# Optimization experiments

Measured on AMD Instinct MI355X. Metric: run time of the kernel, lower is better.

The kernel has to match this reference:

```python
import jax, jax.numpy as jnp
import numpy as np

N = 10000       # n_nodes
E = 640000      # n_edges (avg degree 64)
D_IN = 128      # in_feats
D_H = 128       # n_hidden
N_CLS = 64      # n_classes


def setup_inputs() -> dict:
    key = jax.random.key(0)
    k1, k2, k3, k4, k5, k6 = jax.random.split(key, 6)
    features = jax.random.normal(k1, (N, D_IN), dtype=jnp.float32)
    src = jax.random.randint(k2, (E,), 0, N, dtype=jnp.int32)
    dst = jax.random.randint(k3, (E,), 0, N, dtype=jnp.int32)
    s = 0.05  # small init scale to keep activations bounded across 3 layers
    # Stored as [in, out]; equivalent to torch Linear weight [out, in] transposed.
    W0 = jax.random.normal(k4, (D_IN, D_H), dtype=jnp.float32) * s
    W1 = jax.random.normal(k5, (D_H, D_H), dtype=jnp.float32) * s
    W2 = jax.random.normal(k6, (D_H, N_CLS), dtype=jnp.float32) * s
    return {"features": features, "W0": W0, "W1": W1, "W2": W2,
            "src": src, "dst": dst}


def reference(features, W0, W1, W2, src, dst):
    # GINConv with aggregator 'sum', eps=0 (learn_eps=False):
    #   h' = Linear(h + sum_{(u->v) in E} h[u] scattered to v)
    # Dropout is identity at inference; 'activation' is unused in the module.
    def gin_layer(h, W):
        agg = jax.ops.segment_sum(h[src], dst, num_segments=N)  # [N, d]
        return (h + agg) @ W

    h = gin_layer(features, W0)
    h = gin_layer(h, W1)
    h = gin_layer(h, W2)
    return h
```

## Files before the change

### kernel.cpp

```cpp
#include <hip/hip_runtime.h>
#include <hip/hip_bf16.h>

#define NN 10000
#define NE 640000
#define D_IN 128
#define D_H 128
#define N_CLS 64
#define CAP 160
#define GRP 157
#define CAPC 4800
#define EPB 1024
#define AB 625
#define CB 1251
#define CCS 16

__device__ __forceinline__ float blo(unsigned u) { return __uint_as_float(u << 16); }
__device__ __forceinline__ float bhi(unsigned u) { return __uint_as_float(u & 0xffff0000u); }
__device__ __forceinline__ unsigned short f2bf(float f) {
    unsigned u = __float_as_uint(f);
    return (unsigned short)((u + 0x7fffu + ((u >> 16) & 1u)) >> 16);
}

__global__ __launch_bounds__(256) void prep_a(const int* __restrict__ src,
                                              const int* __restrict__ dst,
                                              int* __restrict__ coarse_cnt,
                                              unsigned* __restrict__ coarse,
                                              const float* __restrict__ feat,
                                              unsigned* __restrict__ hb0) {
    int bid = blockIdx.x;
    if (bid >= AB) {
        int t = (bid - AB) * 256 + threadIdx.x;
        if (t < NN * 32) {
            float4 f = ((const float4*)feat)[t];
            unsigned lo = (unsigned)f2bf(f.x) | ((unsigned)f2bf(f.y) << 16);
            unsigned hi = (unsigned)f2bf(f.z) | ((unsigned)f2bf(f.w) << 16);
            ((uint2*)hb0)[t] = make_uint2(lo, hi);
        } else if (t < (NN + 1) * 32) {
            ((uint2*)hb0)[t] = make_uint2(0u, 0u);
        }
        return;
    }
    __shared__ unsigned stage[EPB];
    __shared__ int hist[GRP], gbase[GRP], cur[GRP];
    const int t = threadIdx.x;
    for (int i = t; i < GRP; i += 256) hist[i] = 0;
    __syncthreads();
    const int e0 = bid * EPB;
    for (int i = t; i < EPB; i += 256) {
        int s = src[e0 + i];
        int d = dst[e0 + i];
        stage[i] = (unsigned)s | ((unsigned)d << 16);
        atomicAdd(&hist[d >> 6], 1);
    }
    __syncthreads();
    for (int i = t; i < GRP; i += 256) {
        gbase[i] = atomicAdd(&coarse_cnt[i * CCS], hist[i]);
        cur[i] = 0;
    }
    __syncthreads();
    for (int i = t; i < EPB; i += 256) {
        unsigned u = stage[i];
        int g = u >> 22;
        int r = atomicAdd(&cur[g], 1);
        coarse[g * CAPC + gbase[g] + r] = u;
    }
}

__global__ __launch_bounds__(1024) void prep_b(const int* __restrict__ coarse_cnt,
                                               const unsigned* __restrict__ coarse,
                                               int* __restrict__ cnt,
                                               unsigned short* __restrict__ colbuf) {
    __shared__ int cur[64];
    const int g = blockIdx.x;
    const int t = threadIdx.x;
    if (t < 64) cur[t] = 0;
    __syncthreads();
    const int m = coarse_cnt[g * CCS];
    const unsigned* cb = coarse + g * CAPC;
    for (int i = t; i < m; i += 1024) {
        unsigned u = cb[i];
        int s = (int)(u & 0xFFFFu);
        int d = (int)(u >> 16);
        int r = atomicAdd(&cur[d - (g << 6)], 1);
        colbuf[d * CAP + r] = (unsigned short)s;
    }
    __syncthreads();
    if (t < 64) {
        int n = (g << 6) + t;
        if (n < NN) {
            int c = cur[t];
            int pad = (4 - (c & 3)) & 3;
            unsigned short* base = colbuf + n * CAP;
            for (int k = 0; k < pad; ++k) base[c + k] = (unsigned short)NN;
            cnt[n] = c + pad;
        }
    }
}

template <int J, int M, bool LAST>
__global__ __launch_bounds__(256) void gin_layer(const uint4* __restrict__ hb4,
                                                 const int* __restrict__ cnt,
                                                 const unsigned short* __restrict__ colbuf,
                                                 const float* __restrict__ W,
                                                 unsigned short* __restrict__ outb,
                                                 float* __restrict__ outf) {
    __shared__ float xs[M][D_H];
    const int base = blockIdx.x * M;
    const int tid = threadIdx.x;
    const int wave = tid >> 6;
    const int lane = tid & 63;
    const int sub = lane >> 4;
    const int off = lane & 15;

#pragma unroll 1
    for (int nm = 0; nm < M / 4; ++nm) {
        const int m = wave + nm * 4;
        const int n = base + m;
        float a0, a1, a2, a3, a4, a5, a6, a7;
        if (sub == 0) {
            uint4 u = hb4[n * 16 + off];
            a0 = blo(u.x); a1 = bhi(u.x); a2 = blo(u.y); a3 = bhi(u.y);
            a4 = blo(u.z); a5 = bhi(u.z); a6 = blo(u.w); a7 = bhi(u.w);
        } else {
            a0 = a1 = a2 = a3 = a4 = a5 = a6 = a7 = 0.f;
        }
        const int G4 = cnt[n] >> 2;
        const uint2* cl8 = (const uint2*)(colbuf + n * CAP);
        int g = 0;
        for (; g + 4 <= G4; g += 4) {
            uint2 p0 = cl8[g + 0];
            uint2 p1 = cl8[g + 1];
            uint2 p2 = cl8[g + 2];
            uint2 p3 = cl8[g + 3];
            unsigned w0 = (sub & 2) ? p0.y : p0.x;
            unsigned w1 = (sub & 2) ? p1.y : p1.x;
            unsigned w2 = (sub & 2) ? p2.y : p2.x;
            unsigned w3 = (sub & 2) ? p3.y : p3.x;
            int s0 = (sub & 1) ? (w0 >> 16) : (w0 & 0xffffu);
            int s1 = (sub & 1) ? (w1 >> 16) : (w1 & 0xffffu);
            int s2 = (sub & 1) ? (w2 >> 16) : (w2 & 0xffffu);
            int s3 = (sub & 1) ? (w3 >> 16) : (w3 & 0xffffu);
            uint4 uA = hb4[s0 * 16 + off];
            uint4 uB = hb4[s1 * 16 + off];
            uint4 uC = hb4[s2 * 16 + off];
            uint4 uD = hb4[s3 * 16 + off];
            a0 += (blo(uA.x) + blo(uB.x)) + (blo(uC.x) + blo(uD.x));
            a1 += (bhi(uA.x) + bhi(uB.x)) + (bhi(uC.x) + bhi(uD.x));
            a2 += (blo(uA.y) + blo(uB.y)) + (blo(uC.y) + blo(uD.y));
            a3 += (bhi(uA.y) + bhi(uB.y)) + (bhi(uC.y) + bhi(uD.y));
            a4 += (blo(uA.z) + blo(uB.z)) + (blo(uC.z) + blo(uD.z));
            a5 += (bhi(uA.z) + bhi(uB.z)) + (bhi(uC.z) + bhi(uD.z));
            a6 += (blo(uA.w) + blo(uB.w)) + (blo(uC.w) + blo(uD.w));
            a7 += (bhi(uA.w) + bhi(uB.w)) + (bhi(uC.w) + bhi(uD.w));
        }
        for (; g < G4; ++g) {
            uint2 p = cl8[g];
            unsigned w = (sub & 2) ? p.y : p.x;
            int s = (sub & 1) ? (w >> 16) : (w & 0xffffu);
            uint4 u = hb4[s * 16 + off];
            a0 += blo(u.x); a1 += bhi(u.x); a2 += blo(u.y); a3 += bhi(u.y);
            a4 += blo(u.z); a5 += bhi(u.z); a6 += blo(u.w); a7 += bhi(u.w);
        }
        a0 += __shfl_xor(a0, 16); a0 += __shfl_xor(a0, 32);
        a1 += __shfl_xor(a1, 16); a1 += __shfl_xor(a1, 32);
        a2 += __shfl_xor(a2, 16); a2 += __shfl_xor(a2, 32);
        a3 += __shfl_xor(a3, 16); a3 += __shfl_xor(a3, 32);
        a4 += __shfl_xor(a4, 16); a4 += __shfl_xor(a4, 32);
        a5 += __shfl_xor(a5, 16); a5 += __shfl_xor(a5, 32);
        a6 += __shfl_xor(a6, 16); a6 += __shfl_xor(a6, 32);
        a7 += __shfl_xor(a7, 16); a7 += __shfl_xor(a7, 32);
        if (sub == 0) {
            *(float4*)&xs[m][8 * off]     = make_float4(a0, a1, a2, a3);
            *(float4*)&xs[m][8 * off + 4] = make_float4(a4, a5, a6, a7);
        }
    }
    __syncthreads();

    constexpr int G = 256 / J;
    constexpr int NM = M / G;
    const int gq = tid / J;
    const int j = tid % J;
    const int mbase = gq * NM;
    float acc[NM];
#pragma unroll
    for (int m = 0; m < NM; ++m) acc[m] = 0.f;

    for (int k = 0; k < D_H; k += 4) {
        float w0 = W[(k + 0) * J + j];
        float w1 = W[(k + 1) * J + j];
        float w2 = W[(k + 2) * J + j];
        float w3 = W[(k + 3) * J + j];
#pragma unroll
        for (int m = 0; m < NM; ++m) {
            float4 xv = *(const float4*)&xs[mbase + m][k];
            acc[m] += xv.x * w0 + xv.y * w1 + xv.z * w2 + xv.w * w3;
        }
    }
#pragma unroll
    for (int m = 0; m < NM; ++m) {
        int n = base + mbase + m;
        if (LAST) __builtin_nontemporal_store(acc[m], &outf[(size_t)n * J + j]);
        else      __builtin_nontemporal_store(f2bf(acc[m]), &outb[(size_t)n * J + j]);
    }
    if (!LAST && blockIdx.x == 0 && tid < 32) {
        ((uint2*)(outb + (size_t)NN * D_H))[tid] = make_uint2(0u, 0u);
    }
}

extern "C" void kernel_launch(void* const* d_in, const int* in_sizes, int n_in,
                              void* d_out, int out_size, void* d_ws, size_t ws_size,
                              hipStream_t stream) {
    const float* features = (const float*)d_in[0];
    const float* W0       = (const float*)d_in[1];
    const float* W1       = (const float*)d_in[2];
    const float* W2       = (const float*)d_in[3];
    const int*   src      = (const int*)d_in[4];
    const int*   dst      = (const int*)d_in[5];
    float* out = (float*)d_out;

    int* coarse_cnt        = (int*)d_ws;
    int* cnt               = coarse_cnt + GRP * CCS;
    unsigned short* colbuf = (unsigned short*)(cnt + NN);
    unsigned* coarse       = (unsigned*)(colbuf + (size_t)NN * CAP);
    unsigned* hb0          = coarse + (size_t)GRP * CAPC;
    unsigned* hb1          = hb0 + (size_t)(NN + 1) * 64;
    unsigned* hb2          = hb1 + (size_t)(NN + 1) * 64;

    hipMemsetAsync(coarse_cnt, 0, GRP * CCS * sizeof(int), stream);
    prep_a<<<AB + CB, 256, 0, stream>>>(src, dst, coarse_cnt, coarse, features, hb0);
    prep_b<<<GRP, 1024, 0, stream>>>(coarse_cnt, coarse, cnt, colbuf);

    constexpr int M = 8;
    gin_layer<D_H, M, false><<<NN / M, 256, 0, stream>>>((const uint4*)hb0, cnt, colbuf, W0,
                                                         (unsigned short*)hb1, nullptr);
    gin_layer<D_H, M, false><<<NN / M, 256, 0, stream>>>((const uint4*)hb1, cnt, colbuf, W1,
                                                         (unsigned short*)hb2, nullptr);
    gin_layer<N_CLS, M, true><<<NN / M, 256, 0, stream>>>((const uint4*)hb2, cnt, colbuf, W2,
                                                          nullptr, out);
}
```

Before: 147.6 us.

## Use bf16-packed weights, one node per wave, and pad neighbor lists to 16

Weights are pre-packed into bf16 pairs inside the prep kernel, which halves weight load traffic in each layer's matmul. Each GIN layer block now handles 4 nodes (one per wave) instead of 8, giving 2500 blocks and requesting higher occupancy through launch bounds. Neighbor lists are padded to multiples of 16 so the unrolled gather loop needs no remainder loop. The trade-offs are more dummy-row gathers, more blocks each reloading the weight matrix, and bf16 rounding of the weights, which adds precision loss.

```diff
diff --git a/kernel.cpp b/kernel.cpp
--- a/kernel.cpp
+++ b/kernel.cpp
@@ -12,6 +12,7 @@
 #define EPB 1024
 #define AB 625
 #define CB 1251
+#define WB 80
 #define CCS 16
 
 __device__ __forceinline__ float blo(unsigned u) { return __uint_as_float(u << 16); }
@@ -20,21 +21,44 @@
     unsigned u = __float_as_uint(f);
     return (unsigned short)((u + 0x7fffu + ((u >> 16) & 1u)) >> 16);
 }
+__device__ __forceinline__ unsigned packbf(float a, float b) {
+    return (unsigned)f2bf(a) | ((unsigned)f2bf(b) << 16);
+}
 
 __global__ __launch_bounds__(256) void prep_a(const int* __restrict__ src,
                                               const int* __restrict__ dst,
                                               int* __restrict__ coarse_cnt,
                                               unsigned* __restrict__ coarse,
                                               const float* __restrict__ feat,
-                                              unsigned* __restrict__ hb0) {
+                                              unsigned* __restrict__ hb0,
+                                              const float* __restrict__ W0,
+                                              const float* __restrict__ W1,
+                                              const float* __restrict__ W2,
+                                              unsigned* __restrict__ wb0,
+                                              unsigned* __restrict__ wb1,
+                                              unsigned* __restrict__ wb2) {
     int bid = blockIdx.x;
+    if (bid >= AB + CB) {
+        int t = (bid - AB - CB) * 256 + threadIdx.x;
+        if (t < 8192) {
+            int kp = t >> 7, j = t & 127;
+            wb0[t] = packbf(W0[(2 * kp) * 128 + j], W0[(2 * kp + 1) * 128 + j]);
+        } else if (t < 16384) {
+            int tt = t - 8192;
+            int kp = tt >> 7, j = tt & 127;
+            wb1[tt] = packbf(W1[(2 * kp) * 128 + j], W1[(2 * kp + 1) * 128 + j]);
+        } else if (t < 20480) {
+            int tt = t - 16384;
+            int kp = tt >> 6, j = tt & 63;
+            wb2[tt] = packbf(W2[(2 * kp) * 64 + j], W2[(2 * kp + 1) * 64 + j]);
+        }
+        return;
+    }
     if (bid >= AB) {
         int t = (bid - AB) * 256 + threadIdx.x;
         if (t < NN * 32) {
             float4 f = ((const float4*)feat)[t];
-            unsigned lo = (unsigned)f2bf(f.x) | ((unsigned)f2bf(f.y) << 16);
-            unsigned hi = (unsigned)f2bf(f.z) | ((unsigned)f2bf(f.w) << 16);
-            ((uint2*)hb0)[t] = make_uint2(lo, hi);
+            ((uint2*)hb0)[t] = make_uint2(packbf(f.x, f.y), packbf(f.z, f.w));
         } else if (t < (NN + 1) * 32) {
             ((uint2*)hb0)[t] = make_uint2(0u, 0u);
         }
@@ -89,7 +113,7 @@
         int n = (g << 6) + t;
         if (n < NN) {
             int c = cur[t];
-            int pad = (4 - (c & 3)) & 3;
+            int pad = (16 - (c & 15)) & 15;
             unsigned short* base = colbuf + n * CAP;
             for (int k = 0; k < pad; ++k) base[c + k] = (unsigned short)NN;
             cnt[n] = c + pad;
@@ -97,13 +121,14 @@
     }
 }
 
-template <int J, int M, bool LAST>
-__global__ __launch_bounds__(256) void gin_layer(const uint4* __restrict__ hb4,
-                                                 const int* __restrict__ cnt,
-                                                 const unsigned short* __restrict__ colbuf,
-                                                 const float* __restrict__ W,
-                                                 unsigned short* __restrict__ outb,
-                                                 float* __restrict__ outf) {
+template <int J, bool LAST>
+__global__ __launch_bounds__(256, 8) void gin_layer(const uint4* __restrict__ hb4,
+                                                    const int* __restrict__ cnt,
+                                                    const unsigned short* __restrict__ colbuf,
+                                                    const unsigned* __restrict__ Wb,
+                                                    unsigned short* __restrict__ outb,
+                                                    float* __restrict__ outf) {
+    constexpr int M = 4;
     __shared__ float xs[M][D_H];
     const int base = blockIdx.x * M;
     const int tid = threadIdx.x;
@@ -112,67 +137,54 @@
     const int sub = lane >> 4;
     const int off = lane & 15;
 
-#pragma unroll 1
-    for (int nm = 0; nm < M / 4; ++nm) {
-        const int m = wave + nm * 4;
-        const int n = base + m;
-        float a0, a1, a2, a3, a4, a5, a6, a7;
-        if (sub == 0) {
-            uint4 u = hb4[n * 16 + off];
-            a0 = blo(u.x); a1 = bhi(u.x); a2 = blo(u.y); a3 = bhi(u.y);
-            a4 = blo(u.z); a5 = bhi(u.z); a6 = blo(u.w); a7 = bhi(u.w);
-        } else {
-            a0 = a1 = a2 = a3 = a4 = a5 = a6 = a7 = 0.f;
-        }
-        const int G4 = cnt[n] >> 2;
-        const uint2* cl8 = (const uint2*)(colbuf + n * CAP);
-        int g = 0;
-        for (; g + 4 <= G4; g += 4) {
-            uint2 p0 = cl8[g + 0];
-            uint2 p1 = cl8[g + 1];
-            uint2 p2 = cl8[g + 2];
-            uint2 p3 = cl8[g + 3];
-            unsigned w0 = (sub & 2) ? p0.y : p0.x;
-            unsigned w1 = (sub & 2) ? p1.y : p1.x;
-            unsigned w2 = (sub & 2) ? p2.y : p2.x;
-            unsigned w3 = (sub & 2) ? p3.y : p3.x;
-            int s0 = (sub & 1) ? (w0 >> 16) : (w0 & 0xffffu);
-            int s1 = (sub & 1) ? (w1 >> 16) : (w1 & 0xffffu);
-            int s2 = (sub & 1) ? (w2 >> 16) : (w2 & 0xffffu);
-            int s3 = (sub & 1) ? (w3 >> 16) : (w3 & 0xffffu);
-            uint4 uA = hb4[s0 * 16 + off];
-            uint4 uB = hb4[s1 * 16 + off];
-            uint4 uC = hb4[s2 * 16 + off];
-            uint4 uD = hb4[s3 * 16 + off];
-            a0 += (blo(uA.x) + blo(uB.x)) + (blo(uC.x) + blo(uD.x));
-            a1 += (bhi(uA.x) + bhi(uB.x)) + (bhi(uC.x) + bhi(uD.x));
-            a2 += (blo(uA.y) + blo(uB.y)) + (blo(uC.y) + blo(uD.y));
-            a3 += (bhi(uA.y) + bhi(uB.y)) + (bhi(uC.y) + bhi(uD.y));
-            a4 += (blo(uA.z) + blo(uB.z)) + (blo(uC.z) + blo(uD.z));
-            a5 += (bhi(uA.z) + bhi(uB.z)) + (bhi(uC.z) + bhi(uD.z));
-            a6 += (blo(uA.w) + blo(uB.w)) + (blo(uC.w) + blo(uD.w));
-            a7 += (bhi(uA.w) + bhi(uB.w)) + (bhi(uC.w) + bhi(uD.w));
-        }
-        for (; g < G4; ++g) {
-            uint2 p = cl8[g];
-            unsigned w = (sub & 2) ? p.y : p.x;
-            int s = (sub & 1) ? (w >> 16) : (w & 0xffffu);
-            uint4 u = hb4[s * 16 + off];
-            a0 += blo(u.x); a1 += bhi(u.x); a2 += blo(u.y); a3 += bhi(u.y);
-            a4 += blo(u.z); a5 += bhi(u.z); a6 += blo(u.w); a7 += bhi(u.w);
-        }
-        a0 += __shfl_xor(a0, 16); a0 += __shfl_xor(a0, 32);
-        a1 += __shfl_xor(a1, 16); a1 += __shfl_xor(a1, 32);
-        a2 += __shfl_xor(a2, 16); a2 += __shfl_xor(a2, 32);
-        a3 += __shfl_xor(a3, 16); a3 += __shfl_xor(a3, 32);
-        a4 += __shfl_xor(a4, 16); a4 += __shfl_xor(a4, 32);
-        a5 += __shfl_xor(a5, 16); a5 += __shfl_xor(a5, 32);
-        a6 += __shfl_xor(a6, 16); a6 += __shfl_xor(a6, 32);
-        a7 += __shfl_xor(a7, 16); a7 += __shfl_xor(a7, 32);
-        if (sub == 0) {
-            *(float4*)&xs[m][8 * off]     = make_float4(a0, a1, a2, a3);
-            *(float4*)&xs[m][8 * off + 4] = make_float4(a4, a5, a6, a7);
-        }
+    const int n = base + wave;
+    float a0, a1, a2, a3, a4, a5, a6, a7;
+    if (sub == 0) {
+        uint4 u = hb4[n * 16 + off];
+        a0 = blo(u.x); a1 = bhi(u.x); a2 = blo(u.y); a3 = bhi(u.y);
+        a4 = blo(u.z); a5 = bhi(u.z); a6 = blo(u.w); a7 = bhi(u.w);
+    } else {
+        a0 = a1 = a2 = a3 = a4 = a5 = a6 = a7 = 0.f;
+    }
+    const int G4 = cnt[n] >> 2;
+    const uint2* cl8 = (const uint2*)(colbuf + n * CAP);
+    for (int g = 0; g < G4; g += 4) {
+        uint2 p0 = cl8[g + 0];
+        uint2 p1 = cl8[g + 1];
+        uint2 p2 = cl8[g + 2];
+        uint2 p3 = cl8[g + 3];
+        unsigned w0 = (sub & 2) ? p0.y : p0.x;
+        unsigned w1 = (sub & 2) ? p1.y : p1.x;
+        unsigned w2 = (sub & 2) ? p2.y : p2.x;
+        unsigned w3 = (sub & 2) ? p3.y : p3.x;
+        int s0 = (sub & 1) ? (w0 >> 16) : (w0 & 0xffffu);
+        int s1 = (sub & 1) ? (w1 >> 16) : (w1 & 0xffffu);
+        int s2 = (sub & 1) ? (w2 >> 16) : (w2 & 0xffffu);
+        int s3 = (sub & 1) ? (w3 >> 16) : (w3 & 0xffffu);
+        uint4 uA = hb4[s0 * 16 + off];
+        uint4 uB = hb4[s1 * 16 + off];
+        uint4 uC = hb4[s2 * 16 + off];
+        uint4 uD = hb4[s3 * 16 + off];
+        a0 += (blo(uA.x) + blo(uB.x)) + (blo(uC.x) + blo(uD.x));
+        a1 += (bhi(uA.x) + bhi(uB.x)) + (bhi(uC.x) + bhi(uD.x));
+        a2 += (blo(uA.y) + blo(uB.y)) + (blo(uC.y) + blo(uD.y));
+        a3 += (bhi(uA.y) + bhi(uB.y)) + (bhi(uC.y) + bhi(uD.y));
+        a4 += (blo(uA.z) + blo(uB.z)) + (blo(uC.z) + blo(uD.z));
+        a5 += (bhi(uA.z) + bhi(uB.z)) + (bhi(uC.z) + bhi(uD.z));
+        a6 += (blo(uA.w) + blo(uB.w)) + (blo(uC.w) + blo(uD.w));
+        a7 += (bhi(uA.w) + bhi(uB.w)) + (bhi(uC.w) + bhi(uD.w));
+    }
+    a0 += __shfl_xor(a0, 16); a0 += __shfl_xor(a0, 32);
+    a1 += __shfl_xor(a1, 16); a1 += __shfl_xor(a1, 32);
+    a2 += __shfl_xor(a2, 16); a2 += __shfl_xor(a2, 32);
+    a3 += __shfl_xor(a3, 16); a3 += __shfl_xor(a3, 32);
+    a4 += __shfl_xor(a4, 16); a4 += __shfl_xor(a4, 32);
+    a5 += __shfl_xor(a5, 16); a5 += __shfl_xor(a5, 32);
+    a6 += __shfl_xor(a6, 16); a6 += __shfl_xor(a6, 32);
+    a7 += __shfl_xor(a7, 16); a7 += __shfl_xor(a7, 32);
+    if (sub == 0) {
+        *(float4*)&xs[wave][8 * off]     = make_float4(a0, a1, a2, a3);
+        *(float4*)&xs[wave][8 * off + 4] = make_float4(a4, a5, a6, a7);
     }
     __syncthreads();
 
@@ -186,10 +198,9 @@
     for (int m = 0; m < NM; ++m) acc[m] = 0.f;
 
     for (int k = 0; k < D_H; k += 4) {
-        float w0 = W[(k + 0) * J + j];
-        float w1 = W[(k + 1) * J + j];
-        float w2 = W[(k + 2) * J + j];
-        float w3 = W[(k + 3) * J + j];
+        unsigned wp0 = Wb[(k >> 1) * J + j];
+        unsigned wp1 = Wb[((k >> 1) + 1) * J + j];
+        float w0 = blo(wp0), w1 = bhi(wp0), w2 = blo(wp1), w3 = bhi(wp1);
 #pragma unroll
         for (int m = 0; m < NM; ++m) {
             float4 xv = *(const float4*)&xs[mbase + m][k];
@@ -198,9 +209,9 @@
     }
 #pragma unroll
     for (int m = 0; m < NM; ++m) {
-        int n = base + mbase + m;
-        if (LAST) __builtin_nontemporal_store(acc[m], &outf[(size_t)n * J + j]);
-        else      __builtin_nontemporal_store(f2bf(acc[m]), &outb[(size_t)n * J + j]);
+        int n2 = base + mbase + m;
+        if (LAST) __builtin_nontemporal_store(acc[m], &outf[(size_t)n2 * J + j]);
+        else      __builtin_nontemporal_store(f2bf(acc[m]), &outb[(size_t)n2 * J + j]);
     }
     if (!LAST && blockIdx.x == 0 && tid < 32) {
         ((uint2*)(outb + (size_t)NN * D_H))[tid] = make_uint2(0u, 0u);
@@ -225,16 +236,19 @@
     unsigned* hb0          = coarse + (size_t)GRP * CAPC;
     unsigned* hb1          = hb0 + (size_t)(NN + 1) * 64;
     unsigned* hb2          = hb1 + (size_t)(NN + 1) * 64;
+    unsigned* wb0          = hb2 + (size_t)(NN + 1) * 64;
+    unsigned* wb1          = wb0 + 8192;
+    unsigned* wb2          = wb1 + 8192;
 
     hipMemsetAsync(coarse_cnt, 0, GRP * CCS * sizeof(int), stream);
-    prep_a<<<AB + CB, 256, 0, stream>>>(src, dst, coarse_cnt, coarse, features, hb0);
+    prep_a<<<AB + CB + WB, 256, 0, stream>>>(src, dst, coarse_cnt, coarse, features, hb0,
+                                             W0, W1, W2, wb0, wb1, wb2);
     prep_b<<<GRP, 1024, 0, stream>>>(coarse_cnt, coarse, cnt, colbuf);
 
-    constexpr int M = 8;
-    gin_layer<D_H, M, false><<<NN / M, 256, 0, stream>>>((const uint4*)hb0, cnt, colbuf, W0,
-                                                         (unsigned short*)hb1, nullptr);
-    gin_layer<D_H, M, false><<<NN / M, 256, 0, stream>>>((const uint4*)hb1, cnt, colbuf, W1,
-                                                         (unsigned short*)hb2, nullptr);
-    gin_layer<N_CLS, M, true><<<NN / M, 256, 0, stream>>>((const uint4*)hb2, cnt, colbuf, W2,
-                                                          nullptr, out);
-}
+    gin_layer<D_H, false><<<NN / 4, 256, 0, stream>>>((const uint4*)hb0, cnt, colbuf, wb0,
+                                                      (unsigned short*)hb1, nullptr);
+    gin_layer<D_H, false><<<NN / 4, 256, 0, stream>>>((const uint4*)hb1, cnt, colbuf, wb1,
+                                                      (unsigned short*)hb2, nullptr);
+    gin_layer<N_CLS, true><<<NN / 4, 256, 0, stream>>>((const uint4*)hb2, cnt, colbuf, wb2,
+                                                       nullptr, out);
+}
```

Measured after the change: 148.4 us. No clear change (+0.5%).
